# Kernel tuning notes

Hardware: AMD Instinct MI355X
Metric: run time of the kernel (lower is better)

Reference implementation:

```python
import jax, jax.numpy as jnp
import numpy as np

_PI = np.pi


def _small_d(l, betas):
    # Wigner small-d: d^l_{m',m}(beta) = <m'| exp(-i beta Jy) |m>, m in [-l..l]
    mvals = np.arange(-l, l + 1)
    dim = 2 * l + 1
    jp = np.zeros((dim, dim))
    for i in range(dim - 1):
        jp[i + 1, i] = np.sqrt(l * (l + 1) - mvals[i] * (mvals[i] + 1))
    Jy = (jp - jp.T) / 2j
    ev, V = np.linalg.eigh(Jy)
    betas = np.atleast_1d(np.asarray(betas, dtype=np.float64))
    ph = np.exp(-1j * betas[:, None] * ev[None, :])
    d = np.einsum('ak,jk,bk->jab', V, ph, V.conj())
    return np.real(d).astype(np.float32)  # [n_beta, 2l+1, 2l+1]


def _dh_weights(b):
    # Driscoll-Healy quadrature weights on beta_j = pi(2j+1)/(4b)
    j = np.arange(2 * b)
    beta = _PI * (2 * j + 1) / (4 * b)
    k = np.arange(b)
    w = (2.0 / b) * np.sin(beta) * np.sum(
        np.sin((2 * k[None, :] + 1) * beta[:, None]) / (2 * k + 1), axis=1)
    return w.astype(np.float32), beta


def _s2_grid(n_alpha, max_beta, n_beta):
    beta = np.arange(1, n_beta + 1) * max_beta / n_beta
    alpha = np.linspace(0, 2 * _PI, n_alpha, endpoint=False)
    Bg, Ag = np.meshgrid(beta, alpha, indexing='ij')
    return Ag.ravel(), Bg.ravel(), np.zeros(Ag.size)


def _so3_grid(n_alpha, max_beta, n_beta, max_gamma, n_gamma):
    beta = np.arange(1, n_beta + 1) * max_beta / n_beta
    alpha = np.linspace(0, 2 * _PI, n_alpha, endpoint=False)
    pre_gamma = np.linspace(-max_gamma, max_gamma, n_gamma, endpoint=False)
    Bg, Ag, Pg = np.meshgrid(beta, alpha, pre_gamma, indexing='ij')
    Cg = Pg - Ag
    return Ag.ravel(), Bg.ravel(), Cg.ravel()


def _make_layer(kind, b_in, b_out, grid):
    a_g, b_g, g_g = grid
    w_in, beta_in = _dh_weights(b_in)
    _, beta_out = _dh_weights(b_out)
    d_in, d_out, psi = [], [], []
    for l in range(b_out):
        din = _small_d(l, beta_in)    # [2b_in, 2l+1, 2l+1]
        dout = _small_d(l, beta_out)  # [2b_out, 2l+1, 2l+1]
        dg = _small_d(l, b_g)         # [P, 2l+1, 2l+1] at kernel-grid betas
        m = np.arange(-l, l + 1)
        if kind == 's2':
            # spherical-harmonic-like basis at grid points: d^l_{m0}(b_p) e^{-i m a_p}
            ps = dg[:, :, l].T * np.exp(-1j * m[:, None] * a_g[None, :])  # [2l+1, P]
        else:
            # Wigner-D basis: e^{-i m a_p} d^l_{mn}(b_p) e^{-i n g_p}
            ps = (np.transpose(dg, (1, 2, 0))
                  * np.exp(-1j * m[:, None, None] * a_g[None, None, :])
                  * np.exp(-1j * m[None, :, None] * g_g[None, None, :]))  # [2l+1,2l+1,P]
        d_in.append(din); d_out.append(dout); psi.append(ps.astype(np.complex64))
    return dict(kind=kind, b_in=b_in, b_out=b_out, w=w_in, d_in=d_in, d_out=d_out, psi=psi)


_LAYERS = [
    _make_layer('s2', 30, 30, _s2_grid(6, _PI / 16, 1)),
    _make_layer('so3', 30, 15, _so3_grid(6, _PI / 16, 1, 2 * _PI, 6)),
    _make_layer('so3', 15, 15, _so3_grid(6, _PI / 8, 1, 2 * _PI, 6)),
    _make_layer('so3', 15, 7, _so3_grid(6, _PI / 8, 1, 2 * _PI, 6)),
    _make_layer('so3', 7, 7, _so3_grid(6, _PI / 4, 1, 2 * _PI, 6)),
    _make_layer('so3', 7, 3, _so3_grid(6, _PI / 4, 1, 2 * _PI, 6)),
    _make_layer('so3', 3, 3, _so3_grid(6, _PI / 2, 1, 2 * _PI, 6)),
]
_W_INT = _dh_weights(3)[0]


def _spectral_conv(x, k, L):
    # S2: x [B,Ci,2b,2b] (beta,alpha); SO3: x [B,Ci,2b,2b,2b] (beta,alpha,gamma)
    kind, b_in, b_out = L['kind'], L['b_in'], L['b_out']
    N_in, N_out = 2 * b_in, 2 * b_out
    Bt, Co = x.shape[0], k.shape[1]
    kc = k.astype(jnp.complex64)
    wq = jnp.asarray(L['w'])
    if kind == 's2':
        xf = jnp.fft.fft(x, axis=-1)            # [B,Ci,beta,m]
    else:
        xf = jnp.fft.fftn(x, axes=(-2, -1))     # [B,Ci,beta,m,n]
    G = jnp.zeros((Bt, Co, N_out, N_out, N_out), jnp.complex64)  # [B,Co,beta',m,n]
    for l in range(b_out):
        m = np.arange(-l, l + 1)
        ii, io = m % N_in, m % N_out
        din = jnp.asarray(L['d_in'][l])
        dout = jnp.asarray(L['d_out'][l]).astype(jnp.complex64)
        psi = jnp.asarray(L['psi'][l])
        if kind == 's2':
            # analysis (GFT) of input and kernel, spectral outer product
            xh = jnp.einsum('j,jm,bcjm->bcm', wq, din[:, :, l], xf[:, :, :, ii])
            yh = jnp.einsum('iop,mp->iom', kc, psi)
            z = jnp.einsum('bim,ion->bomn', xh, jnp.conj(yh))
        else:
            xh = jnp.einsum('j,jmn,bcjmn->bcmn', wq, din,
                            xf[:, :, :, ii[:, None], ii[None, :]])
            yh = jnp.einsum('iop,mnp->iomn', kc, psi)
            z = jnp.einsum('bimk,ionk->bomn', xh, jnp.conj(yh))  # xh yh^dagger
        G = G.at[:, :, :, io[:, None], io[None, :]].add(
            (2 * l + 1) * jnp.einsum('jmn,bomn->bojmn', dout, z))
    # inverse SO3 FFT: Wigner synthesis over beta done above, inverse FFT over (m,n)
    return jnp.real(jnp.fft.ifftn(G, axes=(-2, -1))) * (N_out ** 2)


def _bn(x, g, b):
    mu = x.mean(0)
    var = x.var(0)
    return g * (x - mu) * jax.lax.rsqrt(var + 1e-5) + b


def _forward(x, k1, k2, k3, k4, k5, k6, k7,
             bn_g1, bn_b1, w1, b1, bn_g2, bn_b2, w2, b2, bn_g3, bn_b3, w3, b3):
    h = x
    for kk, L in zip((k1, k2, k3, k4, k5, k6, k7), _LAYERS):
        h = jax.nn.relu(_spectral_conv(h, kk, L))
    # so3_integrate: mean over alpha,gamma, quadrature-weighted sum over beta
    h = jnp.einsum('j,bcj->bc', jnp.asarray(_W_INT), h.mean(axis=(-2, -1)))
    h = jax.nn.relu(_bn(h, bn_g1, bn_b1) @ w1 + b1)
    h = jax.nn.relu(_bn(h, bn_g2, bn_b2) @ w2 + b2)
    return _bn(h, bn_g3, bn_b3) @ w3 + b3


def setup_inputs() -> dict:
    key = jax.random.key(0)
    ks = jax.random.split(key, 16)
    B = 8
    def rn(k, shape, scale=1.0):
        return jax.random.normal(k, shape, dtype=jnp.float32) * scale
    return {
        'x': rn(ks[0], (B, 1, 60, 60)),
        'k1': rn(ks[1], (1, 8, 6), 1.0 / np.sqrt(6)),
        'k2': rn(ks[2], (8, 16, 36), 1.0 / np.sqrt(8 * 36)),
        'k3': rn(ks[3], (16, 16, 36), 1.0 / np.sqrt(16 * 36)),
        'k4': rn(ks[4], (16, 24, 36), 1.0 / np.sqrt(16 * 36)),
        'k5': rn(ks[5], (24, 24, 36), 1.0 / np.sqrt(24 * 36)),
        'k6': rn(ks[6], (24, 32, 36), 1.0 / np.sqrt(24 * 36)),
        'k7': rn(ks[7], (32, 64, 36), 1.0 / np.sqrt(32 * 36)),
        'bn_g1': jnp.ones((64,), jnp.float32), 'bn_b1': jnp.zeros((64,), jnp.float32),
        'w1': rn(ks[8], (64, 64), 0.125), 'b1': jnp.zeros((64,), jnp.float32),
        'bn_g2': jnp.ones((64,), jnp.float32), 'bn_b2': jnp.zeros((64,), jnp.float32),
        'w2': rn(ks[9], (64, 32), 0.125), 'b2': jnp.zeros((32,), jnp.float32),
        'bn_g3': jnp.ones((32,), jnp.float32), 'bn_b3': jnp.zeros((32,), jnp.float32),
        'w3': rn(ks[10], (32, 10), 1.0 / np.sqrt(32)), 'b3': jnp.zeros((10,), jnp.float32),
    }


def reference(x, k1, k2, k3, k4, k5, k6, k7,
              bn_g1, bn_b1, w1, b1, bn_g2, bn_b2, w2, b2, bn_g3, bn_b3, w3, b3):
    return _forward(x, k1, k2, k3, k4, k5, k6, k7,
                    bn_g1, bn_b1, w1, b1, bn_g2, bn_b2, w2, b2, bn_g3, bn_b3, w3, b3)
```

## Files before the change

kernel.cpp:

```cpp
#include <hip/hip_runtime.h>
#include <math.h>


#define DFT_LDS 3712

__host__ __device__ inline long long SF(int l) { return (long long)l * (4LL*l*l - 1) / 3; }
__device__ inline int imod(int a, int n) { int r = a % n; return r < 0 ? r + n : r; }

struct WigCfg {
    int nseg;
    int nblk[16];
    int off[16];
    int b_out[16];
    int colmode[16];
    int jmaj[16];
    int nb[16];
    double beta0[16];
    double bstep[16];
};

__global__ void wigner_all_kernel(float* __restrict__ ws, WigCfg cfg)
{
    __shared__ float lf[128];
    for (int t = threadIdx.x; t < 128; t += blockDim.x)
        lf[t] = (float)lgamma((double)t + 1.0);
    __syncthreads();

    int b = blockIdx.x, s = 0;
    while (b >= cfg.nblk[s]) { b -= cfg.nblk[s]; s++; }
    float* out = ws + cfg.off[s];
    int b_out = cfg.b_out[s];
    int colmode = cfg.colmode[s];
    int jm = cfg.jmaj[s];
    int nb = cfg.nb[s];
    int l = b % b_out, j = b / b_out;
    double beta = cfg.beta0[s] + cfg.bstep[s] * j;

    float x   = (float)cos(beta);
    float lsb = (float)log(sin(0.5 * beta));
    float lcb = (float)log(cos(0.5 * beta));
    int dim = 2*l + 1;
    long long S  = SF(b_out);
    long long Ol = SF(l);
    long long b2 = (long long)b_out * b_out;
    int total = colmode ? dim : dim * dim;
    for (int t = threadIdx.x; t < total; t += blockDim.x) {
        int mi, ni;
        if (colmode) { mi = t; ni = l; }
        else         { mi = t / dim; ni = t % dim; }
        int mp = mi - l, mm = ni - l;
        int k1 = l + mm, k2 = l - mm, k3 = l + mp, k4 = l - mp;
        int kk = min(min(k1, k2), min(k3, k4));
        int a, lam;
        if      (kk == k1) { a = mp - mm; lam = mp - mm; }
        else if (kk == k2) { a = mm - mp; lam = 0; }
        else if (kk == k3) { a = mm - mp; lam = 0; }
        else               { a = mp - mm; lam = mp - mm; }
        int bb = 2*l - 2*kk - a;
        float lpref = 0.5f * (lf[2*l - kk] + lf[kk] - lf[kk + a] - lf[kk + bb]);
        float P = 1.f;
        if (kk >= 1) {
            float fa = (float)a, fb = (float)bb;
            float p0 = 1.f;
            float p1 = 0.5f * ((fa - fb) + (fa + fb + 2.f) * x);
            for (int n = 2; n <= kk; n++) {
                float fn = (float)n;
                float t1 = 2.f*fn + fa + fb;
                float c1 = 2.f*fn*(fn + fa + fb)*(t1 - 2.f);
                float c2 = (t1 - 1.f) * (t1*(t1 - 2.f)*x + fa*fa - fb*fb);
                float c3 = 2.f*(fn + fa - 1.f)*(fn + fb - 1.f)*t1;
                float pn = (c2*p1 - c3*p0) / c1;
                p0 = p1; p1 = pn;
            }
            P = p1;
        }
        float val = expf(lpref + (float)a * lsb + (float)bb * lcb) * P;
        if (lam & 1) val = -val;
        long long e = colmode ? ((long long)l*l + mi) : (Ol + (long long)mi * dim + ni);
        long long idx;
        if (jm) idx = e * nb + j;
        else    idx = colmode ? ((long long)j * b2 + e) : ((long long)j * S + e);
        out[idx] = val;
    }
}

__global__ void setup_kernel(float2* __restrict__ W, float* __restrict__ w)
{
    int t = threadIdx.x + blockIdx.x * blockDim.x;
    if (t >= 110) return;
    const int Ns[4]   = {60, 30, 14, 6};
    const int offs[4] = {0, 60, 90, 104};
    int si = (t < 60) ? 0 : (t < 90) ? 1 : (t < 104) ? 2 : 3;
    int N = Ns[si];
    int k = t - offs[si];
    double ang = -2.0 * M_PI * (double)k / (double)N;
    W[t] = make_float2((float)cos(ang), (float)sin(ang));
    int b = N / 2;
    double beta = M_PI * (2*k + 1) / (4.0 * b);
    double s = 0.0;
    for (int kk = 0; kk < b; kk++) s += sin((2*kk + 1) * beta) / (2*kk + 1);
    w[t] = (float)((2.0 / b) * sin(beta) * s);
}

__global__ void dft_r_kernel(const float* __restrict__ in, float2* __restrict__ out,
                             const float2* __restrict__ Wt,
                             int R, int N, int NF, int RPB)
{
    __shared__ float s[2 * DFT_LDS];
    __shared__ float2 sW[64];
    int r0 = blockIdx.x * RPB;
    if (r0 >= R) return;
    int nr = min(RPB, R - r0);
    for (int t = threadIdx.x; t < N; t += blockDim.x) sW[t] = Wt[t];
    for (int t = threadIdx.x; t < nr * N; t += blockDim.x)
        s[t] = in[(long long)r0 * N + t];
    __syncthreads();
    for (int t = threadIdx.x; t < nr * NF; t += blockDim.x) {
        int rr = t / NF, f = t % NF;
        const float* row = s + rr * N;
        float re = 0.f, im = 0.f;
        int tw = 0;
        for (int n = 0; n < N; n++) {
            float2 w = sW[tw];
            float v = row[n];
            re += v * w.x;
            im += v * w.y;
            tw += f; if (tw >= N) tw -= N;
        }
        out[(long long)(r0 + rr) * NF + f] = make_float2(re, im);
    }
}

__global__ void fft2_kernel(const float* __restrict__ in, float2* __restrict__ out,
                            const float2* __restrict__ Wt,
                            int R, int N, int C2, int SPB)
{
    extern __shared__ float sm[];
    float2* sW = (float2*)sm;
    float*  sIn = sm + 2 * N;
    float2* sMid = (float2*)(sIn + SPB * N * N);
    int tid = threadIdx.x;
    for (int t = tid; t < N; t += 256) sW[t] = Wt[t];
    int s0 = blockIdx.x * SPB;
    int ns = min(SPB, R - s0);
    if (ns <= 0) return;
    int slabIn = N * N;
    for (int t = tid; t < ns * slabIn; t += 256)
        sIn[t] = in[(long long)s0 * slabIn + t];
    __syncthreads();
    int w1 = N * C2;
    for (int t = tid; t < ns * w1; t += 256) {
        int ss = t / w1, p = t - ss * w1;
        int a = p / C2, n = p - a * C2;
        const float* row = sIn + ss * slabIn + a * N;
        float re = 0.f, im = 0.f;
        int tw = 0;
        for (int g = 0; g < N; g++) {
            float2 w = sW[tw];
            float v = row[g];
            re += v * w.x;
            im += v * w.y;
            tw += n; if (tw >= N) tw -= N;
        }
        sMid[ss * w1 + a * C2 + n] = make_float2(re, im);
    }
    __syncthreads();
    int M = 2 * C2 - 1;
    int oslab = C2 * M;
    int w2 = C2 * C2;
    for (int t = tid; t < ns * w2; t += 256) {
        int ss = t / w2, p = t - ss * w2;
        int m = p / C2, npos = p - m * C2;
        const float2* col = sMid + ss * w1 + npos;
        float r1 = 0.f, i1 = 0.f, r2 = 0.f, i2 = 0.f;
        int tw = 0;
        for (int a = 0; a < N; a++) {
            float2 w = sW[tw];
            float2 v = col[a * C2];
            r1 += v.x * w.x - v.y * w.y;
            i1 += v.x * w.y + v.y * w.x;
            r2 += v.x * w.x + v.y * w.y;
            i2 += v.y * w.x - v.x * w.y;
            tw += m; if (tw >= N) tw -= N;
        }
        float2* ob = out + (long long)(s0 + ss) * oslab + (long long)m * M;
        ob[(C2 - 1) + npos] = make_float2(r1, i1);
        if (npos > 0) ob[(C2 - 1) - npos] = make_float2(r2, -i2);
    }
}

__global__ void xh_so3_kernel(const float2* __restrict__ xf, const float* __restrict__ din,
                              const float* __restrict__ wq, float2* __restrict__ xh,
                              int B, int Ci, int Nin, int b_out, int eMul, int jMul)
{
    int l = blockIdx.y;
    int dim = 2*l + 1;
    int M = 2*b_out - 1;
    long long S = SF(b_out), Ol = SF(l);
    int rows = l + 1;
    int total = B * Ci * rows * dim;
    int idx = blockIdx.x * blockDim.x + threadIdx.x;
    if (idx >= total) return;
    int ni  = idx % dim;
    int mip = (idx / dim) % rows;
    int bc  = idx / (dim * rows);
    int mi  = mip + l;
    int mf  = mip;
    int nf  = ni - l + (b_out - 1);
    float re = 0.f, im = 0.f;
    const float2* xb = xf + ((long long)bc * Nin) * b_out * M + (long long)mf * M + nf;
    const float*  db = din + (Ol + (long long)mi * dim + ni) * eMul;
    for (int j = 0; j < Nin; j++) {
        float dv = db[(long long)j * jMul] * wq[j];
        float2 xv = xb[(long long)j * b_out * M];
        re += dv * xv.x; im += dv * xv.y;
    }
    xh[(long long)bc * S + Ol + (long long)mi * dim + ni] = make_float2(re, im);
}

__global__ void xh_s2_kernel(const float2* __restrict__ xf, const float* __restrict__ dincol,
                             const float* __restrict__ wq, float2* __restrict__ xh,
                             int B, int Ci, int Nin, int b_out, int eMul, int jMul)
{
    int l = blockIdx.y;
    int b2 = b_out * b_out;
    int rows = l + 1;
    int total = B * Ci * rows;
    int idx = blockIdx.x * blockDim.x + threadIdx.x;
    if (idx >= total) return;
    int mip = idx % rows;
    int bc  = idx / rows;
    int mi  = mip + l;
    int mf  = mip;
    const float* db = dincol + ((long long)l*l + mi) * eMul;
    float re = 0.f, im = 0.f;
    for (int j = 0; j < Nin; j++) {
        float dv = db[(long long)j * jMul] * wq[j];
        float2 xv = xf[((long long)bc * Nin + j) * b_out + mf];
        re += dv * xv.x; im += dv * xv.y;
    }
    xh[(long long)bc * b2 + (long long)l*l + mi] = make_float2(re, im);
}

__global__ void y_so3_direct(const float* __restrict__ kw, const float* __restrict__ dg,
                             float2* __restrict__ Y, int Ci, int Co, int b_out)
{
    const float cr[6] = {1.f, .5f, -.5f, -1.f, -.5f, .5f};
    const float ci_[6] = {0.f, -0.8660254037844386f, -0.8660254037844386f, 0.f,
                          0.8660254037844386f, 0.8660254037844386f};
    int l = blockIdx.y;
    int dim = 2*l + 1;
    long long Ol = SF(l);
    int Nd = Co * dim;
    int total = Ci * dim * Nd;
    int idx = blockIdx.x * blockDim.x + threadIdx.x;
    if (idx >= total) return;
    int col  = idx % Nd;
    int krow = idx / Nd;
    int ki = krow % dim, i = krow / dim;
    int o  = col / dim,  ni = col % dim;
    float dgv = dg[Ol + (long long)ni * dim + ki];
    int m = ni - l, n = ki - l;
    const float* kb = kw + (long long)(i*Co + o) * 36;
    int step = imod(2 * n, 6);
    float re = 0.f, im = 0.f;
    for (int a = 0; a < 6; a++) {
        int tt = imod(a * (m - n), 6);
        #pragma unroll
        for (int g = 0; g < 6; g++) {
            float kv = kb[a*6 + g];
            re += kv * cr[tt]; im += kv * ci_[tt];
            tt += step; if (tt >= 6) tt -= 6;
        }
    }
    Y[(long long)Ci * Co * Ol + idx] = make_float2(dgv * re, dgv * im);
}

__global__ void z_so3_gemm(const float2* __restrict__ xh, const float2* __restrict__ Y,
                           float2* __restrict__ z, float2* __restrict__ zpart,
                           int B, int Ci, int Co, int b_out, int KS, long long partStride)
{
    int l = b_out - 1 - blockIdx.z;
    int dim = 2*l + 1;
    int rows = l + 1;
    long long S = SF(b_out), Ol = SF(l);
    int Nd = Co * dim;
    int c0 = blockIdx.x * 64;
    if (c0 >= Nd) return;
    int by = blockIdx.y;
    int b  = by % B;
    int kc = by / B;
    int ck = Ci / KS;
    int i0 = kc * ck;
    int tid = threadIdx.x;
    int cc = tid & 63;
    int mg = tid >> 6;
    int col = c0 + cc;
    __shared__ float2 sA[32 * 29];
    __shared__ float2 sY[29 * 64];
    float2 acc[8];
    #pragma unroll
    for (int r = 0; r < 8; r++) acc[r] = make_float2(0.f, 0.f);
    const float2* Yl = Y + (long long)Ci * Co * Ol;
    int rd = rows * dim;
    for (int i = i0; i < i0 + ck; i++) {
        const float2* Ab = xh + ((long long)(b*Ci + i)) * S + Ol + (long long)l * dim;
        for (int t = tid; t < 32 * dim; t += 256)
            sA[t] = (t < rd) ? Ab[t] : make_float2(0.f, 0.f);
        const float2* Yb = Yl + (long long)i * dim * Nd;
        for (int t = tid; t < dim * 64; t += 256) {
            int ki = t >> 6, c = t & 63;
            int gc = c0 + c;
            sY[t] = (gc < Nd) ? Yb[(long long)ki * Nd + gc] : make_float2(0.f, 0.f);
        }
        __syncthreads();
        for (int ki = 0; ki < dim; ki++) {
            float2 y = sY[ki*64 + cc];
            #pragma unroll
            for (int r = 0; r < 8; r++) {
                if (r*4 + mg < rows) {
                    float2 a = sA[(r*4 + mg) * dim + ki];
                    acc[r].x += a.x * y.x + a.y * y.y;
                    acc[r].y += a.y * y.x - a.x * y.y;
                }
            }
        }
        __syncthreads();
    }
    if (col < Nd) {
        float2* zo = (kc == 0) ? z : (zpart + (long long)(kc - 1) * partStride);
        long long base = ((long long)(b*Co + (col / dim))) * S + Ol + (col % dim);
        #pragma unroll
        for (int r = 0; r < 8; r++) {
            int mip = r*4 + mg;
            if (mip < rows) zo[base + (long long)(mip + l) * dim] = acc[r];
        }
    }
}

__global__ void z_reduce(float2* __restrict__ z, const float2* __restrict__ zpart,
                         long long total, long long partStride, int KS)
{
    long long idx = (long long)blockIdx.x * 256 + threadIdx.x;
    if (idx >= total) return;
    float2 a = z[idx];
    for (int k = 0; k < KS - 1; k++) {
        float2 p = zpart[(long long)k * partStride + idx];
        a.x += p.x; a.y += p.y;
    }
    z[idx] = a;
}

__global__ void z_s2_direct(const float2* __restrict__ xh, const float* __restrict__ kw,
                            const float* __restrict__ dg, float2* __restrict__ z,
                            int B, int Ci, int Co, int b_out)
{
    const float cr[6] = {1.f, .5f, -.5f, -1.f, -.5f, .5f};
    const float ci_[6] = {0.f, -0.8660254037844386f, -0.8660254037844386f, 0.f,
                          0.8660254037844386f, 0.8660254037844386f};
    int l = blockIdx.y;
    int dim = 2*l + 1;
    int b2 = b_out * b_out;
    int rows = l + 1;
    long long S = SF(b_out), Ol = SF(l);
    int total = B * Co * rows * dim;
    int idx = blockIdx.x * blockDim.x + threadIdx.x;
    if (idx >= total) return;
    int ni  = idx % dim;
    int mip = (idx / dim) % rows;
    int o   = (idx / (dim * rows)) % Co;
    int b   = idx / (dim * rows * Co);
    int mi  = mip + l;
    float dgv = dg[Ol + (long long)ni * dim + l];
    int m = ni - l;
    int step = imod(m, 6);
    float sre = 0.f, sim = 0.f;
    for (int i = 0; i < Ci; i++) {
        const float* kb = kw + (long long)(i*Co + o) * 6;
        float kre = 0.f, kim = 0.f;
        int tt = 0;
        #pragma unroll
        for (int p = 0; p < 6; p++) {
            float kv = kb[p];
            kre += kv * cr[tt]; kim += kv * ci_[tt];
            tt += step; if (tt >= 6) tt -= 6;
        }
        float2 xv = xh[(long long)(b*Ci + i) * b2 + (long long)l*l + mi];
        sre += xv.x * kre + xv.y * kim;
        sim += xv.y * kre - xv.x * kim;
    }
    z[((long long)(b*Co + o)) * S + Ol + (long long)mi * dim + ni] = make_float2(dgv * sre, dgv * sim);
}

template<int N, int ROWS, int GS, int PPB, int BLK>
__global__ __launch_bounds__(BLK) void synth_t(
    const float2* __restrict__ z, const float* __restrict__ dout,
    const float2* __restrict__ Wt, float* __restrict__ act, int nPlanes)
{
    __shared__ float2 sP1[PPB][ROWS * N];
    __shared__ float2 sW[N];
    int tid = threadIdx.x;
    for (int t = tid; t < N; t += BLK) sW[t] = Wt[t];
    int lane = tid & 63, wave = tid >> 6;
    int sub = lane / GS, g = lane - sub * GS;
    int lp = wave * (64 / GS) + sub;
    int P = blockIdx.x * PPB + lp;
    bool on = (P < nPlanes);
    int bo = on ? (P / N) : 0, j = on ? (P - (P / N) * N) : 0;
    long long S = SF(ROWS);
    const float* dj = dout + (long long)j * S;
    const float2* zb = z + (long long)bo * S;
    float2* P1 = sP1[lp];
    for (int t = g; t < ROWS * N; t += GS) P1[t] = make_float2(0.f, 0.f);
    if (on) {
        for (int l = 0; l < ROWS; l++) {
            int dim = 2*l + 1;
            int run = (l + 1) * dim;
            long long base = SF(l) + (long long)l * dim;
            float fdim = (float)dim;
            float rdim = 1.f / fdim;
            for (int s0 = 0; s0 < run; s0 += GS) {
                int s = s0 + g;
                if (s < run) {
                    int m = (int)((float)s * rdim);
                    int rem = s - m * dim;
                    if (rem < 0)         { m--; rem += dim; }
                    else if (rem >= dim) { m++; rem -= dim; }
                    int q = rem - l; if (q < 0) q += N;
                    long long e = base + s;
                    float dv = dj[e] * fdim;
                    float2 zv = zb[e];
                    float2 cur = P1[m * N + q];
                    cur.x += dv * zv.x; cur.y += dv * zv.y;
                    P1[m * N + q] = cur;
                }
            }
        }
    }
    __syncthreads();
    if (on) {
        for (int t = g; t < ROWS * (N/2); t += GS) {
            int mm = t / (N/2), qp = t - mm * (N/2);
            int row = mm * N;
            float2 a = P1[row + qp];
            float2 b = P1[row + qp + N/2];
            float2 w = sW[qp];
            float2 d = make_float2(a.x - b.x, a.y - b.y);
            P1[row + qp]       = make_float2(a.x + b.x, a.y + b.y);
            P1[row + qp + N/2] = make_float2(d.x * w.x + d.y * w.y,
                                             d.y * w.x - d.x * w.y);
        }
    }
    __syncthreads();
    float2 acc[ROWS];
    #pragma unroll
    for (int m = 0; m < ROWS; m++) acc[m] = make_float2(0.f, 0.f);
    bool act_ = on && (g < N);
    if (act_) {
        int par = g & 1, gp = g >> 1;
        int off = par * (N/2);
        float2 wv = make_float2(1.f, 0.f);
        float2 wg = sW[2 * gp]; wg.y = -wg.y;
        for (int qp = 0; qp < N/2; qp++) {
            #pragma unroll
            for (int m = 0; m < ROWS; m++) {
                float2 v = P1[m * N + off + qp];
                acc[m].x += v.x * wv.x - v.y * wv.y;
                acc[m].y += v.x * wv.y + v.y * wv.x;
            }
            float nx = wv.x * wg.x - wv.y * wg.y;
            wv.y = wv.x * wg.y + wv.y * wg.x;
            wv.x = nx;
        }
    }
    if (!act_) return;
    float* ob = act + ((long long)bo * N + j) * (N * N);
    for (int a = 0; a < N/2; a++) {
        float se = 0.f, so = 0.f;
        int t0 = 0;
        #pragma unroll
        for (int m = 1; m < ROWS; m++) {
            t0 += a; if (t0 >= N) t0 -= N;
            float vx = acc[m].x + acc[m].x;
            float vy = acc[m].y + acc[m].y;
            float2 w0 = sW[t0];
            float term = vx * w0.x + vy * w0.y;
            if (m & 1) so += term; else se += term;
        }
        float base = acc[0].x;
        ob[a * N + g]         = fmaxf(base + se + so, 0.f);
        ob[(a + N/2) * N + g] = fmaxf(base + se - so, 0.f);
    }
}

__global__ __launch_bounds__(256) void synth60_kernel(
    const float2* __restrict__ z, const float* __restrict__ dout,
    const float2* __restrict__ Wt, float* __restrict__ act, int nPlanes)
{
    const int N = 60, ROWS = 30;
    __shared__ float2 sP1[ROWS * N];
    __shared__ float2 sScr[ROWS * N];
    __shared__ float2 sW[N];
    int tid = threadIdx.x;
    for (int t = tid; t < N; t += 256) sW[t] = Wt[t];
    int P = blockIdx.x;
    if (P >= nPlanes) return;
    int bo = P / N, j = P - bo * N;
    long long S = SF(ROWS);
    const float* dj = dout + (long long)j * S;
    const float2* zb = z + (long long)bo * S;

    float2 acc[8];
    int ep[8], esp[8], l0p[8];
    #pragma unroll
    for (int p = 0; p < 8; p++) {
        acc[p] = make_float2(0.f, 0.f);
        int idx = tid + p * 256;
        if (idx < ROWS * N) {
            int m = idx / N, q = idx - m * N;
            int n = (q <= 30) ? q : q - 60;
            int an = (n < 0) ? -n : n;
            int l0 = (m > an) ? m : an;
            l0p[p] = l0;
            esp[p] = 2 * m + 1;
            ep[p]  = m * (2 * l0 + 1) + n + l0;
        } else { l0p[p] = ROWS; esp[p] = 0; ep[p] = 0; }
    }
    if (tid == 0) {
        float d = dj[0];
        float2 zv = zb[0];
        sP1[0] = make_float2(d * zv.x, d * zv.y);
    }
    __syncthreads();
    for (int l = 0; l < ROWS; l++) {
        float2* cur = (l & 1) ? sScr : sP1;
        float2* nxt = (l & 1) ? sP1 : sScr;
        float  dreg[7];
        float2 zreg[7];
        int nld = 0;
        if (l + 1 < ROWS) {
            int l1 = l + 1;
            int dimn1 = 2 * l1 + 1;
            int run1 = (l1 + 1) * dimn1;
            int base1 = l1 * (4 * l1 * l1 - 1) / 3 + l1 * dimn1;
            nld = (run1 > tid) ? ((run1 - tid + 255) >> 8) : 0;
            #pragma unroll
            for (int k = 0; k < 7; k++) {
                if (k < nld) {
                    int t = tid + (k << 8);
                    dreg[k] = dj[base1 + t];
                    zreg[k] = zb[base1 + t];
                }
            }
        }
        float fl = (float)(2 * l + 1);
        #pragma unroll
        for (int p = 0; p < 8; p++) {
            if (l >= l0p[p]) {
                float2 v = cur[ep[p]];
                acc[p].x += fl * v.x; acc[p].y += fl * v.y;
                ep[p] += esp[p];
            }
        }
        #pragma unroll
        for (int k = 0; k < 7; k++) {
            if (k < nld) {
                int t = tid + (k << 8);
                nxt[t] = make_float2(dreg[k] * zreg[k].x, dreg[k] * zreg[k].y);
            }
        }
        __syncthreads();
    }
    #pragma unroll
    for (int p = 0; p < 8; p++) {
        int idx = tid + p * 256;
        if (idx < ROWS * N) sP1[idx] = acc[p];
    }
    __syncthreads();

    for (int t = tid; t < ROWS * 30; t += 256) {
        int mm = t / 30, qp = t - mm * 30;
        int row = mm * N;
        float2 a = sP1[row + qp];
        float2 b = sP1[row + qp + 30];
        float2 w = sW[qp];
        float2 d = make_float2(a.x - b.x, a.y - b.y);
        sP1[row + qp]      = make_float2(a.x + b.x, a.y + b.y);
        sP1[row + qp + 30] = make_float2(d.x * w.x + d.y * w.y,
                                         d.y * w.x - d.x * w.y);
    }
    __syncthreads();
    for (int t = tid; t < ROWS * 30; t += 256) {
        int mm = t / 30, sub = t - mm * 30;
        int h = sub / 15, r = sub - h * 15;
        int base = mm * N + h * 30;
        float2 c0 = sP1[base + r];
        float2 c1 = sP1[base + r + 15];
        float2 w = sW[2 * r];
        float2 d = make_float2(c0.x - c1.x, c0.y - c1.y);
        sP1[base + r]      = make_float2(c0.x + c1.x, c0.y + c1.y);
        sP1[base + r + 15] = make_float2(d.x * w.x + d.y * w.y,
                                         d.y * w.x - d.x * w.y);
    }
    __syncthreads();

    int lane = tid & 63, wave = tid >> 6;
    int g = lane;
    int m0 = wave * 8;
    int cnt = (ROWS - m0 < 8) ? (ROWS - m0) : 8;

    if (g < N) {
        float2 pacc[8];
        #pragma unroll
        for (int mm = 0; mm < 8; mm++) pacc[mm] = make_float2(0.f, 0.f);
        int off = (g & 1) * 30 + ((g >> 1) & 1) * 15;
        float2 wg = sW[4 * (g >> 2)]; wg.y = -wg.y;
        float2 wv = make_float2(1.f, 0.f);
        for (int r = 0; r < 15; r++) {
            #pragma unroll
            for (int mm = 0; mm < 8; mm++) {
                if (mm < cnt) {
                    float2 v = sP1[(m0 + mm) * N + off + r];
                    pacc[mm].x += v.x * wv.x - v.y * wv.y;
                    pacc[mm].y += v.x * wv.y + v.y * wv.x;
                }
            }
            float nx = wv.x * wg.x - wv.y * wg.y;
            wv.y = wv.x * wg.y + wv.y * wg.x;
            wv.x = nx;
        }
        #pragma unroll
        for (int mm = 0; mm < 8; mm++) {
            if (mm < cnt) sP1[(m0 + mm) * N + g] = pacc[mm];
        }
    }
    __syncthreads();

    if (g < N) {
        float bx = sP1[g].x;
        float* ob = act + ((long long)bo * N + j) * (N * N);
        for (int ii = 0; ii < 4; ii++) {
            int a = wave * 4 + ii;
            float se_c = 0.f, se_s = 0.f, so_c = 0.f, so_s = 0.f;
            int t0 = 0;
            #pragma unroll
            for (int m = 1; m < ROWS; m++) {
                t0 += a; if (t0 >= N) t0 -= N;
                float2 w0 = sW[t0];
                float2 v = sP1[m * N + g];
                if (m & 1) { so_c += v.x * w0.x; so_s += v.y * w0.y; }
                else       { se_c += v.x * w0.x; se_s += v.y * w0.y; }
            }
            float ep_ = se_c + se_s, em = se_c - se_s;
            float op_ = so_c + so_s, om = so_c - so_s;
            ob[a * N + g]        = fmaxf(bx + 2.f * (ep_ + op_), 0.f);
            ob[(a + 30) * N + g] = fmaxf(bx + 2.f * (ep_ - op_), 0.f);
            if (a != 0 && a != 15) {
                ob[(30 - a) * N + g] = fmaxf(bx + 2.f * (em - om), 0.f);
                ob[(60 - a) * N + g] = fmaxf(bx + 2.f * (em + om), 0.f);
            }
        }
    }
}

__global__ __launch_bounds__(256) void synth30_kernel(
    const float2* __restrict__ z, const float* __restrict__ dout,
    const float2* __restrict__ Wt, float* __restrict__ act, int nPlanes)
{
    const int N = 30, ROWS = 15;
    __shared__ float2 sStage[2360];
    __shared__ float2 sP1[ROWS * N];
    __shared__ float2 sW[N];
    int tid = threadIdx.x;
    for (int t = tid; t < N; t += 256) sW[t] = Wt[t];
    int P = blockIdx.x;
    if (P >= nPlanes) return;
    int bo = P / N, j = P - bo * N;
    long long S = SF(ROWS);
    const float* dj = dout + (long long)j * S;
    const float2* zb = z + (long long)bo * S;

    for (int l = 0; l < ROWS; l++) {
        int dimn = 2 * l + 1;
        int run  = (l + 1) * dimn;
        int base = l * (4 * l * l - 1) / 3 + l * dimn;
        int so   = l * (4 * l * l + 3 * l - 1) / 6;
        for (int t = tid; t < run; t += 256) {
            float d   = dj[base + t];
            float2 zv = zb[base + t];
            sStage[so + t] = make_float2(d * zv.x, d * zv.y);
        }
    }
    __syncthreads();

    float2 acc[2];
    #pragma unroll
    for (int p = 0; p < 2; p++) {
        acc[p] = make_float2(0.f, 0.f);
        int idx = tid + p * 256;
        if (idx < ROWS * N) {
            int m = idx / N, q = idx - m * N;
            int n = (q <= 15) ? q : q - 30;
            int an = (n < 0) ? -n : n;
            int l0 = (m > an) ? m : an;
            if (l0 < ROWS) {
                int e  = l0 * (4*l0*l0 + 3*l0 - 1) / 6 + m * (2*l0 + 1) + n + l0;
                int de = (l0 + 1) * (2*l0 + 1) + 2*m + 1;
                int dd = 4 * l0 + 5;
                float fl = (float)(2*l0 + 1);
                for (int l = l0; l < ROWS; l++) {
                    float2 v = sStage[e];
                    acc[p].x += fl * v.x; acc[p].y += fl * v.y;
                    e += de; de += dd; dd += 4; fl += 2.f;
                }
            }
        }
    }
    #pragma unroll
    for (int p = 0; p < 2; p++) {
        int idx = tid + p * 256;
        if (idx < ROWS * N) sP1[idx] = acc[p];
    }
    __syncthreads();

    for (int t = tid; t < ROWS * 15; t += 256) {
        int mm = t / 15, qp = t - mm * 15;
        int row = mm * N;
        float2 a = sP1[row + qp];
        float2 b = sP1[row + qp + 15];
        float2 w = sW[qp];
        float2 d = make_float2(a.x - b.x, a.y - b.y);
        sP1[row + qp]      = make_float2(a.x + b.x, a.y + b.y);
        sP1[row + qp + 15] = make_float2(d.x * w.x + d.y * w.y,
                                         d.y * w.x - d.x * w.y);
    }
    __syncthreads();

    int lane = tid & 63, wave = tid >> 6;
    int g = lane;
    int m0 = wave * 4;
    int cnt = (ROWS - m0 < 4) ? (ROWS - m0) : 4;

    if (g < N) {
        float2 pacc[4];
        #pragma unroll
        for (int mm = 0; mm < 4; mm++) pacc[mm] = make_float2(0.f, 0.f);
        int off = (g & 1) * 15;
        float2 wg = sW[2 * (g >> 1)]; wg.y = -wg.y;
        float2 wv = make_float2(1.f, 0.f);
        for (int r = 0; r < 15; r++) {
            #pragma unroll
            for (int mm = 0; mm < 4; mm++) {
                if (mm < cnt) {
                    float2 v = sP1[(m0 + mm) * N + off + r];
                    pacc[mm].x += v.x * wv.x - v.y * wv.y;
                    pacc[mm].y += v.x * wv.y + v.y * wv.x;
                }
            }
            float nx = wv.x * wg.x - wv.y * wg.y;
            wv.y = wv.x * wg.y + wv.y * wg.x;
            wv.x = nx;
        }
        #pragma unroll
        for (int mm = 0; mm < 4; mm++) {
            if (mm < cnt) sP1[(m0 + mm) * N + g] = pacc[mm];
        }
    }
    __syncthreads();

    if (g < N) {
        float bx = sP1[g].x;
        float* ob = act + ((long long)bo * N + j) * (N * N);
        for (int ii = 0; ii < 2; ii++) {
            int a = wave * 2 + ii;
            float se_c = 0.f, se_s = 0.f, so_c = 0.f, so_s = 0.f;
            int t0 = 0;
            #pragma unroll
            for (int m = 1; m < ROWS; m++) {
                t0 += a; if (t0 >= N) t0 -= N;
                float2 w0 = sW[t0];
                float2 v = sP1[m * N + g];
                if (m & 1) { so_c += v.x * w0.x; so_s += v.y * w0.y; }
                else       { se_c += v.x * w0.x; se_s += v.y * w0.y; }
            }
            float ep_ = se_c + se_s, em = se_c - se_s;
            float op_ = so_c + so_s, om = so_c - so_s;
            ob[a * N + g]        = fmaxf(bx + 2.f * (ep_ + op_), 0.f);
            ob[(a + 15) * N + g] = fmaxf(bx + 2.f * (ep_ - op_), 0.f);
            if (a != 0) {
                ob[(15 - a) * N + g] = fmaxf(bx + 2.f * (em - om), 0.f);
                ob[(30 - a) * N + g] = fmaxf(bx + 2.f * (em + om), 0.f);
            }
        }
    }
}

__global__ void integrate_kernel(const float* __restrict__ act,
                                 const float* __restrict__ wq,
                                 float* __restrict__ feat)
{
    int e = blockIdx.x;
    int lane = threadIdx.x;
    const float* base = act + (size_t)e * 216;
    float acc = 0.f;
    for (int i = lane; i < 216; i += 64)
        acc += wq[104 + i / 36] * base[i];
    for (int off = 32; off; off >>= 1) acc += __shfl_down(acc, off);
    if (lane == 0) feat[e] = acc * (1.f / 36.f);
}

__global__ void head_kernel(const float* __restrict__ featg,
    const float* __restrict__ g1, const float* __restrict__ be1,
    const float* __restrict__ w1, const float* __restrict__ b1,
    const float* __restrict__ g2, const float* __restrict__ be2,
    const float* __restrict__ w2, const float* __restrict__ b2,
    const float* __restrict__ g3, const float* __restrict__ be3,
    const float* __restrict__ w3, const float* __restrict__ b3,
    float* __restrict__ out)
{
    __shared__ float feat[512];
    __shared__ float xn[512];
    __shared__ float h1[512];
    __shared__ float h2[256];
    int tid = threadIdx.x;
    for (int t = tid; t < 512; t += blockDim.x) feat[t] = featg[t];
    __syncthreads();
    for (int c = tid; c < 64; c += blockDim.x) {
        float mu = 0.f;
        for (int b = 0; b < 8; b++) mu += feat[b*64 + c];
        mu *= 0.125f;
        float var = 0.f;
        for (int b = 0; b < 8; b++) { float d = feat[b*64 + c] - mu; var += d*d; }
        var *= 0.125f;
        float is = rsqrtf(var + 1e-5f);
        for (int b = 0; b < 8; b++) xn[b*64 + c] = g1[c] * (feat[b*64 + c] - mu) * is + be1[c];
    }
    __syncthreads();
    for (int t = tid; t < 512; t += blockDim.x) {
        int b = t >> 6, o = t & 63;
        float acc = b1[o];
        for (int i = 0; i < 64; i++) acc += xn[b*64 + i] * w1[i*64 + o];
        h1[t] = fmaxf(acc, 0.f);
    }
    __syncthreads();
    for (int c = tid; c < 64; c += blockDim.x) {
        float mu = 0.f;
        for (int b = 0; b < 8; b++) mu += h1[b*64 + c];
        mu *= 0.125f;
        float var = 0.f;
        for (int b = 0; b < 8; b++) { float d = h1[b*64 + c] - mu; var += d*d; }
        var *= 0.125f;
        float is = rsqrtf(var + 1e-5f);
        for (int b = 0; b < 8; b++) xn[b*64 + c] = g2[c] * (h1[b*64 + c] - mu) * is + be2[c];
    }
    __syncthreads();
    for (int t = tid; t < 256; t += blockDim.x) {
        int b = t >> 5, o = t & 31;
        float acc = b2[o];
        for (int i = 0; i < 64; i++) acc += xn[b*64 + i] * w2[i*32 + o];
        h2[t] = fmaxf(acc, 0.f);
    }
    __syncthreads();
    for (int c = tid; c < 32; c += blockDim.x) {
        float mu = 0.f;
        for (int b = 0; b < 8; b++) mu += h2[b*32 + c];
        mu *= 0.125f;
        float var = 0.f;
        for (int b = 0; b < 8; b++) { float d = h2[b*32 + c] - mu; var += d*d; }
        var *= 0.125f;
        float is = rsqrtf(var + 1e-5f);
        for (int b = 0; b < 8; b++) xn[b*32 + c] = g3[c] * (h2[b*32 + c] - mu) * is + be3[c];
    }
    __syncthreads();
    for (int t = tid; t < 80; t += blockDim.x) {
        int b = t / 10, o = t % 10;
        float acc = b3[o];
        for (int i = 0; i < 32; i++) acc += xn[b*32 + i] * w3[i*10 + o];
        out[t] = acc;
    }
}


static inline int hmin(int a, int b) { return a < b ? a : b; }
static inline int hmax(int a, int b) { return a > b ? a : b; }
static inline int twoff(int N) { return N == 60 ? 0 : N == 30 ? 60 : N == 14 ? 90 : 104; }
static inline int wqoffb(int b) { return b == 30 ? 0 : b == 15 ? 60 : b == 7 ? 90 : 104; }

extern "C" void kernel_launch(void* const* d_in, const int* in_sizes, int n_in,
                              void* d_out, int out_size, void* d_ws, size_t ws_size,
                              hipStream_t stream)
{
    (void)in_sizes; (void)n_in; (void)out_size;
    const double PI = 3.14159265358979323846;
    struct LD { int kind, b_in, b_out, Ci, Co; double bg; };
    const LD LAY[7] = {
        {0, 30, 30,  1,  8, PI/16},
        {1, 30, 15,  8, 16, PI/16},
        {1, 15, 15, 16, 16, PI/8},
        {1, 15,  7, 16, 24, PI/8},
        {1,  7,  7, 24, 24, PI/4},
        {1,  7,  3, 24, 32, PI/4},
        {1,  3,  3, 32, 64, PI/2},
    };

    float* ws = (float*)d_ws;
    size_t off = 0;
    auto alloc = [&](size_t n) -> size_t { size_t o = off; off += (n + 63) & ~(size_t)63; return o; };
    size_t oA    = alloc(13400000);
    size_t oB    = alloc(8200000);
    size_t oAct1 = alloc(13824000);
    size_t oAct2 = alloc(3456000);
    size_t oXH   = alloc(1200000);
    size_t oZ    = alloc(4800000);
    size_t oWQ   = alloc(128);
    size_t oTW   = alloc(256);
    size_t oFeat = alloc(512);
    size_t oDin[7], oDout[7], oDg[7];
    for (int i = 0; i < 7; i++) {
        const LD& L = LAY[i];
        long long S = SF(L.b_out);
        bool reuse = (i == 2 || i == 4 || i == 6);
        if (reuse) {
            oDin[i]  = oDout[i-1];
            oDout[i] = oDout[i-1];
        } else {
            size_t din_sz = (L.kind == 0) ? (size_t)(2*L.b_in) * L.b_out * L.b_out
                                          : (size_t)(2*L.b_in) * S;
            oDin[i]  = alloc(din_sz);
            oDout[i] = alloc((size_t)(2*L.b_out) * S);
        }
        oDg[i]   = alloc((size_t)S);
    }
    if ((off + 64) * sizeof(float) > ws_size) return;

    float2* TW = (float2*)(ws + oTW);
    float*  WQ = ws + oWQ;

    setup_kernel<<<1, 128, 0, stream>>>(TW, WQ);

    WigCfg cfg;
    int ns = 0, totBlk = 0;
    auto addSeg = [&](int nblk, size_t o, int b_out, int colmode, int jmaj, int nb,
                      double b0, double bs) {
        cfg.nblk[ns] = nblk; cfg.off[ns] = (int)o; cfg.b_out[ns] = b_out;
        cfg.colmode[ns] = colmode; cfg.jmaj[ns] = jmaj; cfg.nb[ns] = nb;
        cfg.beta0[ns] = b0; cfg.bstep[ns] = bs;
        ns++; totBlk += nblk;
    };
    for (int i = 0; i < 7; i++) {
        const LD& L = LAY[i];
        bool reuse = (i == 2 || i == 4 || i == 6);
        if (!reuse) {
            addSeg(2*L.b_in * L.b_out, oDin[i], L.b_out, (L.kind == 0) ? 1 : 0, 1,
                   2*L.b_in, PI/(4.0*L.b_in), PI/(2.0*L.b_in));
            addSeg(2*L.b_out * L.b_out, oDout[i], L.b_out, 0, 0,
                   2*L.b_out, PI/(4.0*L.b_out), PI/(2.0*L.b_out));
        }
        addSeg(L.b_out, oDg[i], L.b_out, 0, 0, 1, L.bg, 0.0);
    }
    cfg.nseg = ns;
    wigner_all_kernel<<<totBlk, 128, 0, stream>>>(ws, cfg);

    const int Bt = 8;
    const float* cur = (const float*)d_in[0];
    float* actbuf[2] = { ws + oAct1, ws + oAct2 };

    for (int i = 0; i < 7; i++) {
        const LD& L = LAY[i];
        int Nin = 2*L.b_in, Nout = 2*L.b_out, M = 2*L.b_out - 1;
        float2* Bb = (float2*)(ws + oB);
        float2* XH = (float2*)(ws + oXH);
        float2* Z  = (float2*)(ws + oZ);
        const float2* TWin  = TW + twoff(Nin);
        const float2* TWout = TW + twoff(Nout);
        const float*  wql   = WQ + wqoffb(L.b_in);
        const float*  kw    = (const float*)d_in[1 + i];
        float* actOut = actbuf[i & 1];
        bool reuse = (i == 2 || i == 4 || i == 6);
        int eMul = reuse ? 1 : Nin;
        int jMul = reuse ? (int)SF(L.b_out) : 1;

        if (L.kind == 0) {
            int R = Bt * L.Ci * Nin;
            int RPB = hmin(R, hmax(1, 2 * DFT_LDS / Nin));
            dft_r_kernel<<<(R + RPB - 1) / RPB, 256, 0, stream>>>(
                cur, Bb, TWin, R, Nin, L.b_out, RPB);
            int gx = (Bt * L.Ci * L.b_out + 255) / 256;
            xh_s2_kernel<<<dim3(gx, L.b_out), 256, 0, stream>>>(
                Bb, ws + oDin[i], wql, XH, Bt, L.Ci, Nin, L.b_out, eMul, jMul);
            int gz = (Bt * L.Co * L.b_out * M + 255) / 256;
            z_s2_direct<<<dim3(gz, L.b_out), 256, 0, stream>>>(
                XH, kw, ws + oDg[i], Z, Bt, L.Ci, L.Co, L.b_out);
        } else {
            int Rs = Bt * L.Ci * Nin;
            int SPB = (Nin >= 60) ? 1 : (Nin >= 30) ? 2 : (Nin >= 14) ? 8 : 16;
            size_t lds = (size_t)Nin * sizeof(float2)
                       + (size_t)SPB * ((size_t)Nin * Nin * sizeof(float)
                                        + (size_t)Nin * L.b_out * sizeof(float2));
            fft2_kernel<<<(Rs + SPB - 1) / SPB, 256, lds, stream>>>(
                cur, Bb, TWin, Rs, Nin, L.b_out, SPB);
            int gx = (Bt * L.Ci * L.b_out * M + 255) / 256;
            xh_so3_kernel<<<dim3(gx, L.b_out), 256, 0, stream>>>(
                Bb, ws + oDin[i], wql, XH, Bt, L.Ci, Nin, L.b_out, eMul, jMul);
            float2* Yb = (float2*)(ws + oA);
            int ty = L.Ci * M * L.Co * M;
            y_so3_direct<<<dim3((ty + 255) / 256, L.b_out), 256, 0, stream>>>(
                kw, ws + oDg[i], Yb, L.Ci, L.Co, L.b_out);
            const int KS = 4;
            long long partF2 = (long long)Bt * L.Co * SF(L.b_out);
            float2* Zp = (float2*)(ws + oB);
            int ntiles = (L.Co * M + 63) / 64;
            z_so3_gemm<<<dim3(ntiles, Bt * KS, L.b_out), 256, 0, stream>>>(
                XH, Yb, Z, Zp, Bt, L.Ci, L.Co, L.b_out, KS, partF2);
            int rb = (int)((partF2 + 255) / 256);
            z_reduce<<<rb, 256, 0, stream>>>(Z, Zp, partF2, partF2, KS);
        }

        int planes = Bt * L.Co * Nout;
        if (Nout == 60) {
            synth60_kernel<<<planes, 256, 0, stream>>>(Z, ws + oDout[i], TWout, actOut, planes);
        } else if (Nout == 30) {
            synth30_kernel<<<planes, 256, 0, stream>>>(Z, ws + oDout[i], TWout, actOut, planes);
        } else if (Nout == 14) {
            synth_t<14, 7,16,4, 64><<<(planes + 3) / 4,  64, 0, stream>>>(Z, ws + oDout[i], TWout, actOut, planes);
        } else {
            synth_t< 6, 3, 8,8, 64><<<(planes + 7) / 8,  64, 0, stream>>>(Z, ws + oDout[i], TWout, actOut, planes);
        }
        cur = actOut;
    }

    integrate_kernel<<<512, 64, 0, stream>>>(cur, WQ, ws + oFeat);

    head_kernel<<<1, 256, 0, stream>>>(
        ws + oFeat,
        (const float*)d_in[8],  (const float*)d_in[9],  (const float*)d_in[10], (const float*)d_in[11],
        (const float*)d_in[12], (const float*)d_in[13], (const float*)d_in[14], (const float*)d_in[15],
        (const float*)d_in[16], (const float*)d_in[17], (const float*)d_in[18], (const float*)d_in[19],
        (float*)d_out);
}
```

Measured before the change: 1.041 ms.

## Split 60-point synthesis into a G-build kernel and an FFT synthesis kernel

Replaces the fused synth60 kernel, which streamed the Wigner-d and Z coefficients through double-buffered LDS per plane, with a separate g_build60 kernel. That kernel computes the l-summed G[m,n] for all 60 beta values at once, reading Z once per (batch,channel) and the d-table in a j-major transposed layout (jmaj enabled for layer 0's dout). The synthesis kernel then just loads G and does the FFT part. The aim is to remove the redundant per-plane reloading of Z and the per-l barriers. The cost is an extra intermediate buffer round trip through global memory and an extra launch.

```diff
diff --git a/kernel.cpp b/kernel.cpp
--- a/kernel.cpp
+++ b/kernel.cpp
@@ -493,89 +493,59 @@
     }
 }
 
-__global__ __launch_bounds__(256) void synth60_kernel(
-    const float2* __restrict__ z, const float* __restrict__ dout,
-    const float2* __restrict__ Wt, float* __restrict__ act, int nPlanes)
+__global__ __launch_bounds__(512) void g_build60(
+    const float2* __restrict__ z, const float* __restrict__ doutT,
+    float2* __restrict__ G)
+{
+    const int ROWS = 30;
+    const long long S = 35990;
+    int bo  = blockIdx.x;
+    int mq0 = blockIdx.y * 8;
+    int tid = threadIdx.x;
+    int r = tid / 60, j = tid - r * 60;
+    __shared__ float2 sT[480];
+    if (r < 8) {
+        float2 acc = make_float2(0.f, 0.f);
+        int mq = mq0 + r;
+        int m = mq / 60, q = mq - m * 60;
+        int n = (q <= 30) ? q : q - 60;
+        int an = (n < 0) ? -n : n;
+        int l0 = (m > an) ? m : an;
+        if (l0 < ROWS) {
+            const float2* zb = z + (long long)bo * S;
+            int e  = l0*(4*l0*l0 - 1)/3 + (l0 + m)*(2*l0 + 1) + (n + l0);
+            int de = 4*l0*l0 + 8*l0 + 2*m + 5;
+            int dd = 8*l0 + 12;
+            float fl = (float)(2*l0 + 1);
+            for (int l = l0; l < ROWS; l++) {
+                float dv = doutT[(long long)e * 60 + j] * fl;
+                float2 zv = zb[e];
+                acc.x += dv * zv.x; acc.y += dv * zv.y;
+                e += de; de += dd; dd += 8; fl += 2.f;
+            }
+        }
+        sT[j * 8 + r] = acc;
+    }
+    __syncthreads();
+    if (tid < 480) {
+        int j2 = tid >> 3, r2 = tid & 7;
+        G[((long long)(bo * 60 + j2)) * 1800 + mq0 + r2] = sT[tid];
+    }
+}
+
+__global__ __launch_bounds__(256) void synth60b_kernel(
+    const float2* __restrict__ G, const float2* __restrict__ Wt,
+    float* __restrict__ act, int nPlanes)
 {
     const int N = 60, ROWS = 30;
     __shared__ float2 sP1[ROWS * N];
-    __shared__ float2 sScr[ROWS * N];
     __shared__ float2 sW[N];
     int tid = threadIdx.x;
     for (int t = tid; t < N; t += 256) sW[t] = Wt[t];
     int P = blockIdx.x;
     if (P >= nPlanes) return;
-    int bo = P / N, j = P - bo * N;
-    long long S = SF(ROWS);
-    const float* dj = dout + (long long)j * S;
-    const float2* zb = z + (long long)bo * S;
-
-    float2 acc[8];
-    int ep[8], esp[8], l0p[8];
-    #pragma unroll
-    for (int p = 0; p < 8; p++) {
-        acc[p] = make_float2(0.f, 0.f);
-        int idx = tid + p * 256;
-        if (idx < ROWS * N) {
-            int m = idx / N, q = idx - m * N;
-            int n = (q <= 30) ? q : q - 60;
-            int an = (n < 0) ? -n : n;
-            int l0 = (m > an) ? m : an;
-            l0p[p] = l0;
-            esp[p] = 2 * m + 1;
-            ep[p]  = m * (2 * l0 + 1) + n + l0;
-        } else { l0p[p] = ROWS; esp[p] = 0; ep[p] = 0; }
-    }
-    if (tid == 0) {
-        float d = dj[0];
-        float2 zv = zb[0];
-        sP1[0] = make_float2(d * zv.x, d * zv.y);
-    }
-    __syncthreads();
-    for (int l = 0; l < ROWS; l++) {
-        float2* cur = (l & 1) ? sScr : sP1;
-        float2* nxt = (l & 1) ? sP1 : sScr;
-        float  dreg[7];
-        float2 zreg[7];
-        int nld = 0;
-        if (l + 1 < ROWS) {
-            int l1 = l + 1;
-            int dimn1 = 2 * l1 + 1;
-            int run1 = (l1 + 1) * dimn1;
-            int base1 = l1 * (4 * l1 * l1 - 1) / 3 + l1 * dimn1;
-            nld = (run1 > tid) ? ((run1 - tid + 255) >> 8) : 0;
-            #pragma unroll
-            for (int k = 0; k < 7; k++) {
-                if (k < nld) {
-                    int t = tid + (k << 8);
-                    dreg[k] = dj[base1 + t];
-                    zreg[k] = zb[base1 + t];
-                }
-            }
-        }
-        float fl = (float)(2 * l + 1);
-        #pragma unroll
-        for (int p = 0; p < 8; p++) {
-            if (l >= l0p[p]) {
-                float2 v = cur[ep[p]];
-                acc[p].x += fl * v.x; acc[p].y += fl * v.y;
-                ep[p] += esp[p];
-            }
-        }
-        #pragma unroll
-        for (int k = 0; k < 7; k++) {
-            if (k < nld) {
-                int t = tid + (k << 8);
-                nxt[t] = make_float2(dreg[k] * zreg[k].x, dreg[k] * zreg[k].y);
-            }
-        }
-        __syncthreads();
-    }
-    #pragma unroll
-    for (int p = 0; p < 8; p++) {
-        int idx = tid + p * 256;
-        if (idx < ROWS * N) sP1[idx] = acc[p];
-    }
+    const float2* Gp = G + (long long)P * 1800;
+    for (int t = tid; t < ROWS * N; t += 256) sP1[t] = Gp[t];
     __syncthreads();
 
     for (int t = tid; t < ROWS * 30; t += 256) {
@@ -638,7 +608,7 @@
 
     if (g < N) {
         float bx = sP1[g].x;
-        float* ob = act + ((long long)bo * N + j) * (N * N);
+        float* ob = act + (long long)P * (N * N);
         for (int ii = 0; ii < 4; ii++) {
             int a = wave * 4 + ii;
             float se_c = 0.f, se_s = 0.f, so_c = 0.f, so_s = 0.f;
@@ -953,7 +923,7 @@
         if (!reuse) {
             addSeg(2*L.b_in * L.b_out, oDin[i], L.b_out, (L.kind == 0) ? 1 : 0, 1,
                    2*L.b_in, PI/(4.0*L.b_in), PI/(2.0*L.b_in));
-            addSeg(2*L.b_out * L.b_out, oDout[i], L.b_out, 0, 0,
+            addSeg(2*L.b_out * L.b_out, oDout[i], L.b_out, 0, (i == 0) ? 1 : 0,
                    2*L.b_out, PI/(4.0*L.b_out), PI/(2.0*L.b_out));
         }
         addSeg(L.b_out, oDg[i], L.b_out, 0, 0, 1, L.bg, 0.0);
@@ -1018,7 +988,10 @@
 
         int planes = Bt * L.Co * Nout;
         if (Nout == 60) {
-            synth60_kernel<<<planes, 256, 0, stream>>>(Z, ws + oDout[i], TWout, actOut, planes);
+            float2* Gb = (float2*)(ws + oA);
+            g_build60<<<dim3(Bt * L.Co, 225), 512, 0, stream>>>(
+                Z, ws + oDout[i], Gb);
+            synth60b_kernel<<<planes, 256, 0, stream>>>(Gb, TWout, actOut, planes);
         } else if (Nout == 30) {
             synth30_kernel<<<planes, 256, 0, stream>>>(Z, ws + oDout[i], TWout, actOut, planes);
         } else if (Nout == 14) {
```

Result: no change. 1.020 ms (-2.0%).
